# Performance work log

Hardware: AMD Instinct MI355X
Metric: run time of the kernel (lower is better)

## Reference

```python
import jax, jax.numpy as jnp
import numpy as np

NUM_CLASSES = 19
COUNT = 6
EPS = 1e-5


def setup_inputs() -> dict:
    key = jax.random.key(0)
    k1, k2 = jax.random.split(key)
    x = jax.random.normal(k1, (4, 256, 256, 256), dtype=jnp.float32)  # [B, C, H, W]
    y = jax.random.randint(k2, (4, 256, 256), 0, NUM_CLASSES)          # [B, H, W]
    return {"x": x, "y": y}


def reference(x, y):
    # Faithful vectorized version of the per-class masked mean/std loop:
    # means[b,k,c] = mean of x[b,c] over pixels with y[b]==k   (if count>COUNT else 0)
    # stds[b,k,c]  = unbiased std over those pixels + eps      (if count>COUNT else 0)
    B, C, H, W = x.shape
    N = H * W
    xf = x.reshape(B, C, N)                     # [B, C, N]
    yf = y.reshape(B, N)                        # [B, N]
    # one-hot segment membership; labels like 255 simply match no class
    onehot = (yf[:, None, :] == jnp.arange(NUM_CLASSES)[None, :, None]).astype(x.dtype)  # [B, K, N]
    cnt = onehot.sum(-1)                        # [B, K]
    s = jnp.einsum('bkn,bcn->bkc', onehot, xf)          # per-class sum
    ss = jnp.einsum('bkn,bcn->bkc', onehot, xf * xf)    # per-class sum of squares
    valid = cnt > COUNT                         # [B, K]
    vm = valid[..., None]                       # [B, K, 1]
    cnt_safe = jnp.maximum(cnt, 1.0)[..., None]
    mean = s / cnt_safe
    # unbiased variance: (sum(x^2) - n*mean^2) / (n-1)
    denom = jnp.maximum(cnt - 1.0, 1.0)[..., None]
    var = jnp.maximum((ss - cnt[..., None] * mean * mean) / denom, 0.0)
    std = jnp.sqrt(jnp.where(vm, var, 1.0)) + EPS
    means = jnp.where(vm, mean, 0.0)
    stds = jnp.where(vm, std, 0.0)
    return means, stds, valid
```

## Files before the change

kernel.cpp:

```cpp
#include <hip/hip_runtime.h>

#define NCLS 19
#define NCH 256
#define NPIX 65536
#define NBATCH 4
#define TPB 256
#define EPSV 1e-5f
#define CNT_THRESH 6

__global__ __launch_bounds__(TPB) void count_kernel(const int* __restrict__ y,
                                                    int* __restrict__ counts,
                                                    float* __restrict__ valid_out) {
    __shared__ int h[NCLS][TPB];
    const int tid = threadIdx.x;
    const int b = blockIdx.x;
    for (int k = 0; k < NCLS; ++k) h[k][tid] = 0;
    __syncthreads();
    const int4* yp = (const int4*)(y + (size_t)b * NPIX);
    #pragma unroll 4
    for (int it = 0; it < NPIX / (TPB * 4); ++it) {
        int4 l = yp[it * TPB + tid];
        if ((unsigned)l.x < NCLS) h[l.x][tid]++;
        if ((unsigned)l.y < NCLS) h[l.y][tid]++;
        if ((unsigned)l.z < NCLS) h[l.z][tid]++;
        if ((unsigned)l.w < NCLS) h[l.w][tid]++;
    }
    for (int s = TPB / 2; s > 0; s >>= 1) {
        __syncthreads();
        if (tid < s)
            for (int k = 0; k < NCLS; ++k) h[k][tid] += h[k][tid + s];
    }
    __syncthreads();
    if (tid < NCLS) {
        int n = h[tid][0];
        counts[b * NCLS + tid] = n;
        valid_out[b * NCLS + tid] = (n > CNT_THRESH) ? 1.0f : 0.0f;
    }
}

__global__ __launch_bounds__(TPB) void moment_kernel(const float* __restrict__ x,
                                                     const int* __restrict__ y,
                                                     const int* __restrict__ counts,
                                                     float* __restrict__ out) {
    __shared__ float2 acc[NCLS][TPB];
    const int tid = threadIdx.x;
    const int c = blockIdx.x;
    const int b = blockIdx.y;

    for (int k = 0; k < NCLS; ++k) acc[k][tid] = make_float2(0.f, 0.f);
    __syncthreads();

    const float4* xp = (const float4*)(x + ((size_t)(b * NCH + c)) * NPIX);
    const int4*   yp = (const int4*)(y + (size_t)b * NPIX);

    for (int it = 0; it < NPIX / (TPB * 4); ++it) {
        const int idx = it * TPB + tid;
        float4 v = xp[idx];
        int4   l = yp[idx];
        if ((unsigned)l.x < NCLS) { float2 t = acc[l.x][tid]; t.x += v.x; t.y = fmaf(v.x, v.x, t.y); acc[l.x][tid] = t; }
        if ((unsigned)l.y < NCLS) { float2 t = acc[l.y][tid]; t.x += v.y; t.y = fmaf(v.y, v.y, t.y); acc[l.y][tid] = t; }
        if ((unsigned)l.z < NCLS) { float2 t = acc[l.z][tid]; t.x += v.z; t.y = fmaf(v.z, v.z, t.y); acc[l.z][tid] = t; }
        if ((unsigned)l.w < NCLS) { float2 t = acc[l.w][tid]; t.x += v.w; t.y = fmaf(v.w, v.w, t.y); acc[l.w][tid] = t; }
    }

    for (int s = TPB / 2; s > 0; s >>= 1) {
        __syncthreads();
        if (tid < s) {
            for (int k = 0; k < NCLS; ++k) {
                float2 a = acc[k][tid];
                float2 o = acc[k][tid + s];
                a.x += o.x; a.y += o.y;
                acc[k][tid] = a;
            }
        }
    }
    __syncthreads();

    if (tid < NCLS) {
        const int k = tid;
        const float n = (float)counts[b * NCLS + k];
        const bool valid = n > (float)CNT_THRESH;
        float2 t = acc[k][0];
        float mean = t.x / fmaxf(n, 1.0f);
        float denom = fmaxf(n - 1.0f, 1.0f);
        float var = fmaxf((t.y - n * mean * mean) / denom, 0.0f);
        float m_out = valid ? mean : 0.0f;
        float s_out = valid ? (sqrtf(var) + EPSV) : 0.0f;
        const int o = (b * NCLS + k) * NCH + c;
        out[o] = m_out;
        out[NBATCH * NCLS * NCH + o] = s_out;
    }
}

extern "C" void kernel_launch(void* const* d_in, const int* in_sizes, int n_in,
                              void* d_out, int out_size, void* d_ws, size_t ws_size,
                              hipStream_t stream) {
    const float* x = (const float*)d_in[0];
    const int*   y = (const int*)d_in[1];
    float* out = (float*)d_out;
    int* counts = (int*)d_ws;
    float* valid_out = out + 2 * NBATCH * NCLS * NCH;

    count_kernel<<<NBATCH, TPB, 0, stream>>>(y, counts, valid_out);

    dim3 grid(NCH, NBATCH);
    moment_kernel<<<grid, TPB, 0, stream>>>(x, y, counts, out);
}
```

Baseline: 422.3 us.

## Fuse class counting into moment kernel with wave-lane LDS atomics

Drops the separate count kernel and computes per-class counts inside the moment kernel, so there is one launch and no workspace dependency. Per-thread LDS histograms (19x256 float2) are replaced by a compact 3x20x64 layout shared by the four waves and updated with LDS float atomics. Invalid labels are clamped into a dump row 19 instead of being branched on. The tree reduction with many __syncthreads becomes wave shuffles. Atomics add contention across the four waves and a third accumulator per pixel, while cutting LDS footprint, which may raise occupancy.

Result: slower. 1.255 ms (+197.2%).

```diff
diff --git a/kernel.cpp b/kernel.cpp
--- a/kernel.cpp
+++ b/kernel.cpp
@@ -1,6 +1,8 @@
 #include <hip/hip_runtime.h>
 
 #define NCLS 19
+#define NROW 20
+#define NLANE 64
 #define NCH 256
 #define NPIX 65536
 #define NBATCH 4
@@ -8,87 +10,67 @@
 #define EPSV 1e-5f
 #define CNT_THRESH 6
 
-__global__ __launch_bounds__(TPB) void count_kernel(const int* __restrict__ y,
-                                                    int* __restrict__ counts,
-                                                    float* __restrict__ valid_out) {
-    __shared__ int h[NCLS][TPB];
-    const int tid = threadIdx.x;
-    const int b = blockIdx.x;
-    for (int k = 0; k < NCLS; ++k) h[k][tid] = 0;
-    __syncthreads();
-    const int4* yp = (const int4*)(y + (size_t)b * NPIX);
-    #pragma unroll 4
-    for (int it = 0; it < NPIX / (TPB * 4); ++it) {
-        int4 l = yp[it * TPB + tid];
-        if ((unsigned)l.x < NCLS) h[l.x][tid]++;
-        if ((unsigned)l.y < NCLS) h[l.y][tid]++;
-        if ((unsigned)l.z < NCLS) h[l.z][tid]++;
-        if ((unsigned)l.w < NCLS) h[l.w][tid]++;
-    }
-    for (int s = TPB / 2; s > 0; s >>= 1) {
-        __syncthreads();
-        if (tid < s)
-            for (int k = 0; k < NCLS; ++k) h[k][tid] += h[k][tid + s];
-    }
-    __syncthreads();
-    if (tid < NCLS) {
-        int n = h[tid][0];
-        counts[b * NCLS + tid] = n;
-        valid_out[b * NCLS + tid] = (n > CNT_THRESH) ? 1.0f : 0.0f;
-    }
-}
-
 __global__ __launch_bounds__(TPB) void moment_kernel(const float* __restrict__ x,
                                                      const int* __restrict__ y,
-                                                     const int* __restrict__ counts,
                                                      float* __restrict__ out) {
-    __shared__ float2 acc[NCLS][TPB];
-    const int tid = threadIdx.x;
+    __shared__ float acc[3][NROW][NLANE];
+    const int tid  = threadIdx.x;
+    const int lane = tid & 63;
     const int c = blockIdx.x;
     const int b = blockIdx.y;
 
-    for (int k = 0; k < NCLS; ++k) acc[k][tid] = make_float2(0.f, 0.f);
+    for (int i = tid; i < 3 * NROW * NLANE; i += TPB) ((float*)acc)[i] = 0.f;
     __syncthreads();
 
     const float4* xp = (const float4*)(x + ((size_t)(b * NCH + c)) * NPIX);
     const int4*   yp = (const int4*)(y + (size_t)b * NPIX);
 
+    #pragma unroll 4
     for (int it = 0; it < NPIX / (TPB * 4); ++it) {
         const int idx = it * TPB + tid;
         float4 v = xp[idx];
         int4   l = yp[idx];
-        if ((unsigned)l.x < NCLS) { float2 t = acc[l.x][tid]; t.x += v.x; t.y = fmaf(v.x, v.x, t.y); acc[l.x][tid] = t; }
-        if ((unsigned)l.y < NCLS) { float2 t = acc[l.y][tid]; t.x += v.y; t.y = fmaf(v.y, v.y, t.y); acc[l.y][tid] = t; }
-        if ((unsigned)l.z < NCLS) { float2 t = acc[l.z][tid]; t.x += v.z; t.y = fmaf(v.z, v.z, t.y); acc[l.z][tid] = t; }
-        if ((unsigned)l.w < NCLS) { float2 t = acc[l.w][tid]; t.x += v.w; t.y = fmaf(v.w, v.w, t.y); acc[l.w][tid] = t; }
-    }
-
-    for (int s = TPB / 2; s > 0; s >>= 1) {
-        __syncthreads();
-        if (tid < s) {
-            for (int k = 0; k < NCLS; ++k) {
-                float2 a = acc[k][tid];
-                float2 o = acc[k][tid + s];
-                a.x += o.x; a.y += o.y;
-                acc[k][tid] = a;
-            }
-        }
+        int k0 = min((unsigned)l.x, (unsigned)NCLS);
+        int k1 = min((unsigned)l.y, (unsigned)NCLS);
+        int k2 = min((unsigned)l.z, (unsigned)NCLS);
+        int k3 = min((unsigned)l.w, (unsigned)NCLS);
+        unsafeAtomicAdd(&acc[0][k0][lane], v.x);
+        unsafeAtomicAdd(&acc[1][k0][lane], v.x * v.x);
+        unsafeAtomicAdd(&acc[2][k0][lane], 1.0f);
+        unsafeAtomicAdd(&acc[0][k1][lane], v.y);
+        unsafeAtomicAdd(&acc[1][k1][lane], v.y * v.y);
+        unsafeAtomicAdd(&acc[2][k1][lane], 1.0f);
+        unsafeAtomicAdd(&acc[0][k2][lane], v.z);
+        unsafeAtomicAdd(&acc[1][k2][lane], v.z * v.z);
+        unsafeAtomicAdd(&acc[2][k2][lane], 1.0f);
+        unsafeAtomicAdd(&acc[0][k3][lane], v.w);
+        unsafeAtomicAdd(&acc[1][k3][lane], v.w * v.w);
+        unsafeAtomicAdd(&acc[2][k3][lane], 1.0f);
     }
     __syncthreads();
 
-    if (tid < NCLS) {
-        const int k = tid;
-        const float n = (float)counts[b * NCLS + k];
-        const bool valid = n > (float)CNT_THRESH;
-        float2 t = acc[k][0];
-        float mean = t.x / fmaxf(n, 1.0f);
-        float denom = fmaxf(n - 1.0f, 1.0f);
-        float var = fmaxf((t.y - n * mean * mean) / denom, 0.0f);
-        float m_out = valid ? mean : 0.0f;
-        float s_out = valid ? (sqrtf(var) + EPSV) : 0.0f;
-        const int o = (b * NCLS + k) * NCH + c;
-        out[o] = m_out;
-        out[NBATCH * NCLS * NCH + o] = s_out;
+    const int w = tid >> 6;
+    for (int k = w; k < NCLS; k += 4) {
+        float s = acc[0][k][lane];
+        float q = acc[1][k][lane];
+        float n = acc[2][k][lane];
+        for (int off = 32; off > 0; off >>= 1) {
+            s += __shfl_down(s, off);
+            q += __shfl_down(q, off);
+            n += __shfl_down(n, off);
+        }
+        if (lane == 0) {
+            const bool valid = n > (float)CNT_THRESH;
+            float mean = s / fmaxf(n, 1.0f);
+            float var  = fmaxf((q - n * mean * mean) / fmaxf(n - 1.0f, 1.0f), 0.0f);
+            float m_out = valid ? mean : 0.0f;
+            float s_out = valid ? (sqrtf(var) + EPSV) : 0.0f;
+            const int o = (b * NCLS + k) * NCH + c;
+            out[o] = m_out;
+            out[NBATCH * NCLS * NCH + o] = s_out;
+            if (c == 0)
+                out[2 * NBATCH * NCLS * NCH + b * NCLS + k] = valid ? 1.0f : 0.0f;
+        }
     }
 }
 
@@ -98,11 +80,7 @@
     const float* x = (const float*)d_in[0];
     const int*   y = (const int*)d_in[1];
     float* out = (float*)d_out;
-    int* counts = (int*)d_ws;
-    float* valid_out = out + 2 * NBATCH * NCLS * NCH;
-
-    count_kernel<<<NBATCH, TPB, 0, stream>>>(y, counts, valid_out);
 
     dim3 grid(NCH, NBATCH);
-    moment_kernel<<<grid, TPB, 0, stream>>>(x, y, counts, out);
+    moment_kernel<<<grid, TPB, 0, stream>>>(x, y, out);
 }
```
